# Kernel tuning notes

Measured on AMD Instinct MI355X. Metric: run time of the kernel, lower is better.

## Reference

```python
import jax, jax.numpy as jnp
import numpy as np

D_MODEL = 1024
NUM_HEADS = 16
HEAD_DIM = D_MODEL // NUM_HEADS
B, S = 2, 2048
EPS = 1e-8


def setup_inputs() -> dict:
    key = jax.random.key(0)
    ks = jax.random.split(key, 9)
    sc = 1.0 / np.sqrt(D_MODEL)
    return {
        "x": jax.random.normal(ks[0], (B, S, D_MODEL), jnp.float32),
        "wq": jax.random.normal(ks[1], (D_MODEL, D_MODEL), jnp.float32) * sc,
        "bq": jax.random.normal(ks[2], (D_MODEL,), jnp.float32) * 0.01,
        "wk": jax.random.normal(ks[3], (D_MODEL, D_MODEL), jnp.float32) * sc,
        "bk": jax.random.normal(ks[4], (D_MODEL,), jnp.float32) * 0.01,
        "wv": jax.random.normal(ks[5], (D_MODEL, D_MODEL), jnp.float32) * sc,
        "bv": jax.random.normal(ks[6], (D_MODEL,), jnp.float32) * 0.01,
        "wo": jax.random.normal(ks[7], (D_MODEL, D_MODEL), jnp.float32) * sc,
        "bo": jax.random.normal(ks[8], (D_MODEL,), jnp.float32) * 0.01,
    }


def reference(x, wq, bq, wk, bk, wv, bv, wo, bo):
    b, s, d = x.shape
    h, hd = NUM_HEADS, HEAD_DIM
    # projections (torch Linear: y = x W^T + b); reshape to [b, h, s, hd]
    def proj(w, bias):
        return (jnp.einsum('bsd,ed->bse', x, w) + bias).reshape(b, s, h, hd).transpose(0, 2, 1, 3)
    q = proj(wq, bq)
    k = proj(wk, bk)
    v = proj(wv, bv)
    scores = jnp.einsum('bhqd,bhkd->bhqk', q, k) / np.sqrt(hd)
    attn = jax.nn.softmax(scores, axis=-1)
    o = jnp.einsum('bhqk,bhkd->bhqd', attn, v)  # [b, h, s, hd]
    # per-position, per-head Gram-Schmidt exclusion: remove component of o[i]
    # along v[i] (the loop in the original is independent over positions)
    v_norm_sq = jnp.sum(v * v, axis=-1, keepdims=True)          # [b,h,s,1]
    align = jnp.sum(o * v, axis=-1, keepdims=True) / (v_norm_sq + EPS)
    o = o - align * v
    o = o.transpose(0, 2, 1, 3).reshape(b, s, d)
    return jnp.einsum('bsd,ed->bse', o, wo) + bo
```

## Files before the change

kernel.cpp:

```cpp
#include <hip/hip_runtime.h>
#include <stdint.h>

#define SEQ 2048
#define NTOK 4096
#define DM 1024

typedef __bf16 bf16x8 __attribute__((ext_vector_type(8)));
typedef __bf16 bf16x4 __attribute__((ext_vector_type(4)));
typedef float f32x4 __attribute__((ext_vector_type(4)));

__device__ __forceinline__ unsigned short f2bf(float f) {
  union { float f; unsigned u; } v; v.f = f;
  return (unsigned short)((v.u + 0x7fffu + ((v.u >> 16) & 1u)) >> 16);
}
__device__ __forceinline__ float bf2f(unsigned short s) {
  union { unsigned u; float f; } v; v.u = ((unsigned)s) << 16; return v.f;
}
__device__ __forceinline__ unsigned pkbf(float a, float b) {
  union { float f; unsigned u; } x, y; x.f = a; y.f = b;
  return __builtin_amdgcn_perm(y.u + 0x8000u, x.u + 0x8000u, 0x07060302u);
}

__device__ __forceinline__ void async16(const unsigned short* g, unsigned short* l) {
  __builtin_amdgcn_global_load_lds(
      (const __attribute__((address_space(1))) void*)g,
      (__attribute__((address_space(3))) void*)l, 16, 0, 0);
}

__global__ __launch_bounds__(256) void cast_all(
    const float* __restrict__ x, const float* __restrict__ wq,
    const float* __restrict__ wk, const float* __restrict__ wv,
    const float* __restrict__ wo, unsigned short* __restrict__ dst) {
  size_t i = ((size_t)blockIdx.x * 256 + threadIdx.x) * 4;
  const float* src; size_t off;
  if (i < (size_t)NTOK * DM) { src = x; off = i; }
  else {
    size_t j = i - (size_t)NTOK * DM;
    int s = (int)(j >> 20);
    src = (s == 0) ? wq : (s == 1) ? wk : (s == 2) ? wv : wo;
    off = j & 1048575u;
  }
  float4 f = *(const float4*)(src + off);
  ushort4 o;
  o.x = f2bf(f.x); o.y = f2bf(f.y); o.z = f2bf(f.z); o.w = f2bf(f.w);
  *(ushort4*)(dst + i) = o;
}


template<int MI>
__device__ __forceinline__ void stage_half(
    const unsigned short* __restrict__ A, const unsigned short* __restrict__ Bw,
    int m0, int n0, int kt, unsigned short* As, unsigned short* Bs) {
  const int tid = threadIdx.x;
  const int r = tid >> 2, c = tid & 3;
#pragma unroll
  for (int b = 0; b < MI / 2; ++b) {
    const int row = b * 64 + r;
    async16(A + (size_t)(m0 + row) * 1024 + kt + ((c ^ (row & 3)) << 3),
            As + row * 32 + c * 8);
  }
#pragma unroll
  for (int b = 0; b < 2; ++b) {
    const int row = b * 64 + r;
    async16(Bw + (size_t)(n0 + row) * 1024 + kt + ((c ^ (row & 3)) << 3),
            Bs + row * 32 + c * 8);
  }
}

__device__ __forceinline__ void pipe_bar0() {
  asm volatile("s_waitcnt vmcnt(0)\ns_barrier" ::: "memory");
}
template<int MI>
__device__ __forceinline__ void pipe_barN() {
  if constexpr (MI == 4) asm volatile("s_waitcnt vmcnt(4)\ns_barrier" ::: "memory");
  else                   asm volatile("s_waitcnt vmcnt(3)\ns_barrier" ::: "memory");
}

template<int MI>
__device__ __forceinline__ void gemm_pipe(
    const unsigned short* __restrict__ A, const unsigned short* __restrict__ Bw,
    int m0, int n0, f32x4 (&acc)[MI][4],
    unsigned short* AsBase, unsigned short* BsBase) {
  const int tid = threadIdx.x, lane = tid & 63, w = tid >> 6;
  const int wm16 = (w >> 1) * MI * 16, wn = (w & 1) * 64;
  const int quad = lane >> 4, l16 = lane & 15;
  constexpr int ASZ = MI * 32 * 32;
  constexpr int BSZ = 128 * 32;

  stage_half<MI>(A, Bw, m0, n0, 0,  AsBase,       BsBase);
  stage_half<MI>(A, Bw, m0, n0, 32, AsBase + ASZ, BsBase + BSZ);
  pipe_barN<MI>();

  int cur = 0;
  for (int p = 0; p < 32; ++p) {
    const unsigned short* As = AsBase + cur * ASZ;
    const unsigned short* Bs = BsBase + cur * BSZ;

    bf16x8 af[MI], bf[4];
    const int swz = ((quad ^ (l16 & 3)) << 3);
#pragma unroll
    for (int i = 0; i < MI; ++i)
      af[i] = *(const bf16x8*)(As + (wm16 + i * 16 + l16) * 32 + swz);
#pragma unroll
    for (int j = 0; j < 4; ++j)
      bf[j] = *(const bf16x8*)(Bs + (wn + j * 16 + l16) * 32 + swz);

    if (p + 2 < 32) {
      const int slot = (cur == 0) ? 2 : cur - 1;
      stage_half<MI>(A, Bw, m0, n0, (p + 2) * 32,
                     AsBase + slot * ASZ, BsBase + slot * BSZ);
    }

#pragma unroll
    for (int i = 0; i < MI; ++i)
#pragma unroll
      for (int j = 0; j < 4; ++j)
        acc[i][j] = __builtin_amdgcn_mfma_f32_16x16x32_bf16(af[i], bf[j], acc[i][j], 0, 0, 0);

    if (p < 30)       pipe_barN<MI>();
    else if (p == 30) pipe_bar0();
    cur = (cur == 2) ? 0 : cur + 1;
  }
}

__global__ __launch_bounds__(256, 3) void qkv_gemm(
    const unsigned short* __restrict__ xb,
    const unsigned short* __restrict__ wqb, const unsigned short* __restrict__ wkb,
    const unsigned short* __restrict__ wvb,
    const float* __restrict__ bq, const float* __restrict__ bk, const float* __restrict__ bv,
    unsigned short* __restrict__ Q, unsigned short* __restrict__ Kd,
    unsigned short* __restrict__ Vt) {
  __shared__ unsigned short As[3 * 128 * 32], Bs[3 * 128 * 32];
  const int gx = blockIdx.x;
  const int kind = gx >> 8;
  const int rr = gx & 255;
  const int tok = 4 * (rr & 7) + ((rr >> 3) & 3);
  const int oth = rr >> 5;
  const unsigned short* A; const unsigned short* Bw;
  int m0, n0;
  if (kind == 2) { A = wvb; Bw = xb; m0 = oth * 128; n0 = tok * 128; }
  else { A = xb; Bw = kind ? wkb : wqb; m0 = tok * 128; n0 = oth * 128; }

  f32x4 acc[4][4];
#pragma unroll
  for (int i = 0; i < 4; ++i)
#pragma unroll
    for (int j = 0; j < 4; ++j) { f32x4 z = {0.f, 0.f, 0.f, 0.f}; acc[i][j] = z; }
  gemm_pipe<4>(A, Bw, m0, n0, acc, As, Bs);

  const int lane = threadIdx.x & 63, w = threadIdx.x >> 6;
  const int quad = lane >> 4, l16 = lane & 15;
  const int wm = (w >> 1) * 64, wn = (w & 1) * 64;

  if (kind == 2) {
#pragma unroll
    for (int i = 0; i < 4; ++i)
#pragma unroll
      for (int j = 0; j < 4; ++j) {
        const int n = n0 + wn + j * 16 + l16;
        const int tb = n >> 11, s = n & 2047;
#pragma unroll
        for (int r = 0; r < 4; ++r) {
          const int m = m0 + wm + i * 16 + quad * 4 + r;
          const int h = m >> 6, d = m & 63;
          Vt[((size_t)(tb * 16 + h) * 64 + d) * SEQ + s] = f2bf(acc[i][j][r] + bv[m]);
        }
      }
  } else {
    const float* bias = (kind == 0) ? bq : bk;
    const float scale = (kind == 0) ? 0.180336880f : 1.0f;
#pragma unroll
    for (int i = 0; i < 4; ++i)
#pragma unroll
      for (int j = 0; j < 4; ++j) {
        const int col = n0 + wn + j * 16 + l16;
        const float bb = bias[col];
        const int h = col >> 6, d = col & 63;
#pragma unroll
        for (int r = 0; r < 4; ++r) {
          const int m = m0 + wm + i * 16 + quad * 4 + r;
          const int b = m >> 11, s = m & 2047;
          const int bh = b * 16 + h;
          const unsigned short val = f2bf((acc[i][j][r] + bb) * scale);
          if (kind == 0) Q[((size_t)bh * SEQ + s) * 64 + d] = val;
          else           Kd[((size_t)bh * SEQ + s) * 64 + d] = val;
        }
      }
  }
}

__global__ __launch_bounds__(256, 4) void attn_kernel(
    const unsigned short* __restrict__ Q, const unsigned short* __restrict__ Kd,
    const unsigned short* __restrict__ Vt,
    unsigned short* __restrict__ Op, float* __restrict__ Lp) {
  __shared__ unsigned short KV[4][4096];
  const int gx = blockIdx.x;
  const int xcd = gx & 7;
  const int idx = gx >> 3;
  const int bh  = xcd * 4 + (idx & 3);
  const int ksl = (idx >> 2) & 1;
  const int q0  = (idx >> 3) * 128;
  const int ks0 = ksl << 10;
  const int tid = threadIdx.x, lane = tid & 63, w = tid >> 6;
  const int quad = lane >> 4, l16 = lane & 15;
  const unsigned short* Qp = Q + (size_t)bh * SEQ * 64;
  const unsigned short* Kp = Kd + (size_t)bh * SEQ * 64;
  const unsigned short* Vp = Vt + (size_t)bh * 64 * SEQ;
  const int srow = tid >> 3;
  const int sc = ((tid & 7) ^ ((srow & 3) | ((srow & 8) >> 1))) << 3;

#pragma unroll
  for (int c = 0; c < 4; ++c)
    async16(Qp + (size_t)(q0 + c * 32 + srow) * 64 + sc,
            KV[c >> 1] + (c & 1) * 2048 + tid * 8);
  __syncthreads();

  const int gl = (l16 & 3) | ((l16 & 8) >> 1);
  const int sel = l16 & 7;
  const unsigned short* Qsrc = KV[w >> 1] + (w & 1) * 2048;
  bf16x8 bQ[2][2];
#pragma unroll
  for (int qq = 0; qq < 2; ++qq) {
    const int qrow = qq * 16 + l16;
#pragma unroll
    for (int hh = 0; hh < 2; ++hh)
      bQ[qq][hh] = *(const bf16x8*)(Qsrc + qrow * 64 + (((hh * 4 + quad) ^ gl) << 3));
  }
  __syncthreads();

  async16(Kp + (size_t)(ks0 + srow) * 64 + sc, KV[0] + tid * 8);
  async16(Kp + (size_t)(ks0 + 32 + srow) * 64 + sc, KV[0] + 2048 + tid * 8);
  async16(Vp + (size_t)srow * SEQ + ks0 + sc, KV[2] + tid * 8);
  async16(Vp + (size_t)(32 + srow) * SEQ + ks0 + sc, KV[2] + 2048 + tid * 8);

  union { unsigned short u[8]; bf16x8 v; } one8;
#pragma unroll
  for (int t = 0; t < 8; ++t) one8.u[t] = 0x3F80;
  const bf16x8 aOnes = one8.v;

  f32x4 o_acc[2][4];
  f32x4 l_acc[2];
  const f32x4 zinit = {-12.f, -12.f, -12.f, -12.f};
#pragma unroll
  for (int qq = 0; qq < 2; ++qq) {
    f32x4 z = {0.f, 0.f, 0.f, 0.f};
    l_acc[qq] = z;
#pragma unroll
    for (int dt = 0; dt < 4; ++dt) o_acc[qq][dt] = z;
  }

  for (int it = 0; it < 16; ++it) {
    const int cur = it & 1;
    __syncthreads();
    if (it + 1 < 16) {
      const int kt = ks0 + (it + 1) * 64, nb = (it + 1) & 1;
      async16(Kp + (size_t)(kt + srow) * 64 + sc, KV[nb] + tid * 8);
      async16(Kp + (size_t)(kt + 32 + srow) * 64 + sc, KV[nb] + 2048 + tid * 8);
      async16(Vp + (size_t)srow * SEQ + kt + sc, KV[2 + nb] + tid * 8);
      async16(Vp + (size_t)(32 + srow) * SEQ + kt + sc, KV[2 + nb] + 2048 + tid * 8);
    }
    const unsigned short* Ks = KV[cur];
    const unsigned short* Vs = KV[2 + cur];

    bf16x8 bP[2][2];
#pragma unroll
    for (int ee = 0; ee < 4; ++ee) {
      const int G = ee >> 1, e = ee & 1;
      const int R = G * 32 + ((l16 >> 2) << 3) + e * 4 + (l16 & 3);
      const unsigned short* arow = Ks + R * 64;
      bf16x8 a0 = *(const bf16x8*)(arow + ((quad ^ sel) << 3));
      bf16x8 a1 = *(const bf16x8*)(arow + (((4 + quad) ^ sel) << 3));
#pragma unroll
      for (int qq = 0; qq < 2; ++qq) {
        f32x4 z = __builtin_amdgcn_mfma_f32_16x16x32_bf16(a0, bQ[qq][0], zinit, 0, 0, 0);
        z = __builtin_amdgcn_mfma_f32_16x16x32_bf16(a1, bQ[qq][1], z, 0, 0, 0);
        const unsigned u0 = (unsigned)(int)__builtin_fmaf(z[0], 8388608.0f, 1065024977.0f);
        const unsigned u1 = (unsigned)(int)__builtin_fmaf(z[1], 8388608.0f, 1065024977.0f);
        const unsigned u2 = (unsigned)(int)__builtin_fmaf(z[2], 8388608.0f, 1065024977.0f);
        const unsigned u3 = (unsigned)(int)__builtin_fmaf(z[3], 8388608.0f, 1065024977.0f);
        union { unsigned d[4]; bf16x8 v; } pk;
        pk.v = bP[qq][G];
        pk.d[e * 2]     = __builtin_amdgcn_perm(u1, u0, 0x07060302u);
        pk.d[e * 2 + 1] = __builtin_amdgcn_perm(u3, u2, 0x07060302u);
        bP[qq][G] = pk.v;
      }
    }

#pragma unroll
    for (int qq = 0; qq < 2; ++qq)
#pragma unroll
      for (int G = 0; G < 2; ++G)
        l_acc[qq] = __builtin_amdgcn_mfma_f32_16x16x32_bf16(aOnes, bP[qq][G], l_acc[qq], 0, 0, 0);

#pragma unroll
    for (int dt = 0; dt < 4; ++dt) {
      const unsigned short* vbase = Vs + (dt * 16 + l16) * 64;
#pragma unroll
      for (int G = 0; G < 2; ++G) {
        bf16x8 aV = *(const bf16x8*)(vbase + (((G * 4 + quad) ^ gl) << 3));
#pragma unroll
        for (int qq = 0; qq < 2; ++qq)
          o_acc[qq][dt] = __builtin_amdgcn_mfma_f32_16x16x32_bf16(aV, bP[qq][G], o_acc[qq][dt], 0, 0, 0);
      }
    }
  }

  const size_t sb = (size_t)(ksl * 32 + bh);
#pragma unroll
  for (int qq = 0; qq < 2; ++qq) {
    const int qg = q0 + w * 32 + qq * 16 + l16;
#pragma unroll
    for (int dt = 0; dt < 4; ++dt)
#pragma unroll
      for (int r = 0; r < 4; ++r) {
        const int d = dt * 16 + quad * 4 + r;
        Op[(sb * 64 + d) * SEQ + qg] = f2bf(o_acc[qq][dt][r]);
      }
    if (quad == 0) Lp[sb * SEQ + qg] = l_acc[qq][0];
  }
}

__global__ __launch_bounds__(128) void combine_kernel(
    const unsigned short* __restrict__ Op, const float* __restrict__ Lp,
    const unsigned short* __restrict__ Vt, unsigned short* __restrict__ O) {
  const int bh = blockIdx.y;
  const int q = blockIdx.x * 128 + threadIdx.x;
  const size_t QC = (size_t)32 * SEQ;
  const size_t idx = (size_t)bh * SEQ + q;
  const float inv = 1.0f / (Lp[idx] + Lp[QC + idx]);
  const unsigned short* O1 = Op + (size_t)bh * 64 * SEQ + q;
  const unsigned short* O2 = O1 + QC * 64;
  const unsigned short* Vp = Vt + (size_t)bh * 64 * SEQ + q;
  float o64[64];
  float ov = 0.f, vv = 0.f;
#pragma unroll
  for (int d = 0; d < 64; ++d) {
    const float o = (bf2f(O1[(size_t)d * SEQ]) + bf2f(O2[(size_t)d * SEQ])) * inv;
    const float v = bf2f(Vp[(size_t)d * SEQ]);
    o64[d] = o; ov += o * v; vv += v * v;
  }
  const float align = ov / (vv + 1e-8f);
  const int b = bh >> 4, h = bh & 15;
  unsigned short* dst = O + (size_t)(b * SEQ + q) * DM + h * 64;
#pragma unroll
  for (int d = 0; d < 64; d += 2) {
    const float a0 = o64[d]     - align * bf2f(Vp[(size_t)d * SEQ]);
    const float a1 = o64[d + 1] - align * bf2f(Vp[(size_t)(d + 1) * SEQ]);
    *(unsigned*)(dst + d) = pkbf(a0, a1);
  }
}

__global__ __launch_bounds__(256) void out_gemm(
    const unsigned short* __restrict__ Ob, const unsigned short* __restrict__ wob,
    const float* __restrict__ bo, float* __restrict__ out) {
  __shared__ unsigned short As[3 * 64 * 32], Bs[3 * 128 * 32];
  const int m0 = blockIdx.y * 64, n0 = blockIdx.x * 128;
  f32x4 acc[2][4];
#pragma unroll
  for (int i = 0; i < 2; ++i)
#pragma unroll
    for (int j = 0; j < 4; ++j) { f32x4 z = {0.f, 0.f, 0.f, 0.f}; acc[i][j] = z; }

  gemm_pipe<2>(Ob, wob, m0, n0, acc, As, Bs);

  const int lane = threadIdx.x & 63, w = threadIdx.x >> 6;
  const int quad = lane >> 4, l16 = lane & 15;
  const int wm = (w >> 1) * 32, wn = (w & 1) * 64;
#pragma unroll
  for (int i = 0; i < 2; ++i)
#pragma unroll
    for (int j = 0; j < 4; ++j) {
      const int col = n0 + wn + j * 16 + l16;
      const float bb = bo[col];
#pragma unroll
      for (int r = 0; r < 4; ++r) {
        const int m = m0 + wm + i * 16 + quad * 4 + r;
        out[(size_t)m * DM + col] = acc[i][j][r] + bb;
      }
    }
}

extern "C" void kernel_launch(void* const* d_in, const int* in_sizes, int n_in,
                              void* d_out, int out_size, void* d_ws, size_t ws_size,
                              hipStream_t stream) {
  const float* x  = (const float*)d_in[0];
  const float* wq = (const float*)d_in[1];
  const float* bq = (const float*)d_in[2];
  const float* wk = (const float*)d_in[3];
  const float* bk = (const float*)d_in[4];
  const float* wv = (const float*)d_in[5];
  const float* bv = (const float*)d_in[6];
  const float* wo = (const float*)d_in[7];
  const float* bo = (const float*)d_in[8];
  float* out = (float*)d_out;
  (void)in_sizes; (void)n_in; (void)out_size; (void)ws_size;

  unsigned short* ws  = (unsigned short*)d_ws;
  unsigned short* xb  = ws;
  unsigned short* wqb = xb + (size_t)NTOK * DM;
  unsigned short* wkb = wqb + (size_t)DM * DM;
  unsigned short* wvb = wkb + (size_t)DM * DM;
  unsigned short* wob = wvb + (size_t)DM * DM;
  unsigned short* Qb  = wob + (size_t)DM * DM;
  unsigned short* Kb  = Qb + (size_t)NTOK * DM;
  unsigned short* Vtb = Kb + (size_t)NTOK * DM;
  unsigned short* Ob  = Vtb + (size_t)NTOK * DM;
  unsigned short* Opb = Ob + (size_t)NTOK * DM;
  float* Lpw = (float*)(Opb + (size_t)2 * 32 * 64 * SEQ);

  cast_all<<<8192, 256, 0, stream>>>(x, wq, wk, wv, wo, ws);
  qkv_gemm<<<768, 256, 0, stream>>>(xb, wqb, wkb, wvb, bq, bk, bv, Qb, Kb, Vtb);
  attn_kernel<<<1024, 256, 0, stream>>>(Qb, Kb, Vtb, Opb, Lpw);
  combine_kernel<<<dim3(16, 32), 128, 0, stream>>>(Opb, Lpw, Vtb, Ob);
  out_gemm<<<dim3(8, 64), 256, 0, stream>>>(Ob, wob, bo, out);
}
```

Baseline: 187.7 us.

## Double query tile per attention block and triple-buffer K/V staging

```diff
diff --git a/kernel.cpp b/kernel.cpp
--- a/kernel.cpp
+++ b/kernel.cpp
@@ -189,17 +189,17 @@
   }
 }
 
-__global__ __launch_bounds__(256, 4) void attn_kernel(
+__global__ __launch_bounds__(256, 3) void attn_kernel(
     const unsigned short* __restrict__ Q, const unsigned short* __restrict__ Kd,
     const unsigned short* __restrict__ Vt,
     unsigned short* __restrict__ Op, float* __restrict__ Lp) {
-  __shared__ unsigned short KV[4][4096];
+  __shared__ unsigned short KK[3][4096], VV[3][4096];
   const int gx = blockIdx.x;
   const int xcd = gx & 7;
   const int idx = gx >> 3;
   const int bh  = xcd * 4 + (idx & 3);
   const int ksl = (idx >> 2) & 1;
-  const int q0  = (idx >> 3) * 128;
+  const int q0  = (idx >> 3) * 256;
   const int ks0 = ksl << 10;
   const int tid = threadIdx.x, lane = tid & 63, w = tid >> 6;
   const int quad = lane >> 4, l16 = lane & 15;
@@ -210,17 +210,19 @@
   const int sc = ((tid & 7) ^ ((srow & 3) | ((srow & 8) >> 1))) << 3;
 
 #pragma unroll
-  for (int c = 0; c < 4; ++c)
-    async16(Qp + (size_t)(q0 + c * 32 + srow) * 64 + sc,
-            KV[c >> 1] + (c & 1) * 2048 + tid * 8);
+  for (int c = 0; c < 8; ++c) {
+    unsigned short* qd = (c < 6) ? (KK[c >> 1] + (c & 1) * 2048)
+                                 : (VV[0] + (c & 1) * 2048);
+    async16(Qp + (size_t)(q0 + c * 32 + srow) * 64 + sc, qd + tid * 8);
+  }
   __syncthreads();
 
   const int gl = (l16 & 3) | ((l16 & 8) >> 1);
   const int sel = l16 & 7;
-  const unsigned short* Qsrc = KV[w >> 1] + (w & 1) * 2048;
-  bf16x8 bQ[2][2];
-#pragma unroll
-  for (int qq = 0; qq < 2; ++qq) {
+  const unsigned short* Qsrc = (w < 3) ? KK[w] : VV[0];
+  bf16x8 bQ[4][2];
+#pragma unroll
+  for (int qq = 0; qq < 4; ++qq) {
     const int qrow = qq * 16 + l16;
 #pragma unroll
     for (int hh = 0; hh < 2; ++hh)
@@ -228,41 +230,40 @@
   }
   __syncthreads();
 
-  async16(Kp + (size_t)(ks0 + srow) * 64 + sc, KV[0] + tid * 8);
-  async16(Kp + (size_t)(ks0 + 32 + srow) * 64 + sc, KV[0] + 2048 + tid * 8);
-  async16(Vp + (size_t)srow * SEQ + ks0 + sc, KV[2] + tid * 8);
-  async16(Vp + (size_t)(32 + srow) * SEQ + ks0 + sc, KV[2] + 2048 + tid * 8);
+  auto stageKV = [&](int j, int slot) {
+    const int kt = ks0 + j * 64;
+    async16(Kp + (size_t)(kt + srow) * 64 + sc, KK[slot] + tid * 8);
+    async16(Kp + (size_t)(kt + 32 + srow) * 64 + sc, KK[slot] + 2048 + tid * 8);
+    async16(Vp + (size_t)srow * SEQ + kt + sc, VV[slot] + tid * 8);
+    async16(Vp + (size_t)(32 + srow) * SEQ + kt + sc, VV[slot] + 2048 + tid * 8);
+  };
+  stageKV(0, 0);
+  stageKV(1, 1);
+  asm volatile("s_waitcnt vmcnt(4)\ns_barrier" ::: "memory");
 
   union { unsigned short u[8]; bf16x8 v; } one8;
 #pragma unroll
   for (int t = 0; t < 8; ++t) one8.u[t] = 0x3F80;
   const bf16x8 aOnes = one8.v;
 
-  f32x4 o_acc[2][4];
-  f32x4 l_acc[2];
+  f32x4 o_acc[4][4];
+  f32x4 l_acc[4];
   const f32x4 zinit = {-12.f, -12.f, -12.f, -12.f};
 #pragma unroll
-  for (int qq = 0; qq < 2; ++qq) {
+  for (int qq = 0; qq < 4; ++qq) {
     f32x4 z = {0.f, 0.f, 0.f, 0.f};
     l_acc[qq] = z;
 #pragma unroll
     for (int dt = 0; dt < 4; ++dt) o_acc[qq][dt] = z;
   }
 
+  int cur = 0;
   for (int it = 0; it < 16; ++it) {
-    const int cur = it & 1;
-    __syncthreads();
-    if (it + 1 < 16) {
-      const int kt = ks0 + (it + 1) * 64, nb = (it + 1) & 1;
-      async16(Kp + (size_t)(kt + srow) * 64 + sc, KV[nb] + tid * 8);
-      async16(Kp + (size_t)(kt + 32 + srow) * 64 + sc, KV[nb] + 2048 + tid * 8);
-      async16(Vp + (size_t)srow * SEQ + kt + sc, KV[2 + nb] + tid * 8);
-      async16(Vp + (size_t)(32 + srow) * SEQ + kt + sc, KV[2 + nb] + 2048 + tid * 8);
-    }
-    const unsigned short* Ks = KV[cur];
-    const unsigned short* Vs = KV[2 + cur];
-
-    bf16x8 bP[2][2];
+    if (it + 2 < 16) stageKV(it + 2, (cur == 0) ? 2 : cur - 1);
+    const unsigned short* Ks = KK[cur];
+    const unsigned short* Vs = VV[cur];
+
+    bf16x8 bP[4][2];
 #pragma unroll
     for (int ee = 0; ee < 4; ++ee) {
       const int G = ee >> 1, e = ee & 1;
@@ -271,7 +272,7 @@
       bf16x8 a0 = *(const bf16x8*)(arow + ((quad ^ sel) << 3));
       bf16x8 a1 = *(const bf16x8*)(arow + (((4 + quad) ^ sel) << 3));
 #pragma unroll
-      for (int qq = 0; qq < 2; ++qq) {
+      for (int qq = 0; qq < 4; ++qq) {
         f32x4 z = __builtin_amdgcn_mfma_f32_16x16x32_bf16(a0, bQ[qq][0], zinit, 0, 0, 0);
         z = __builtin_amdgcn_mfma_f32_16x16x32_bf16(a1, bQ[qq][1], z, 0, 0, 0);
         const unsigned u0 = (unsigned)(int)__builtin_fmaf(z[0], 8388608.0f, 1065024977.0f);
@@ -287,7 +288,7 @@
     }
 
 #pragma unroll
-    for (int qq = 0; qq < 2; ++qq)
+    for (int qq = 0; qq < 4; ++qq)
 #pragma unroll
       for (int G = 0; G < 2; ++G)
         l_acc[qq] = __builtin_amdgcn_mfma_f32_16x16x32_bf16(aOnes, bP[qq][G], l_acc[qq], 0, 0, 0);
@@ -299,16 +300,20 @@
       for (int G = 0; G < 2; ++G) {
         bf16x8 aV = *(const bf16x8*)(vbase + (((G * 4 + quad) ^ gl) << 3));
 #pragma unroll
-        for (int qq = 0; qq < 2; ++qq)
+        for (int qq = 0; qq < 4; ++qq)
           o_acc[qq][dt] = __builtin_amdgcn_mfma_f32_16x16x32_bf16(aV, bP[qq][G], o_acc[qq][dt], 0, 0, 0);
       }
     }
+
+    if (it < 14)       asm volatile("s_waitcnt vmcnt(4)\ns_barrier" ::: "memory");
+    else if (it == 14) asm volatile("s_waitcnt vmcnt(0)\ns_barrier" ::: "memory");
+    cur = (cur == 2) ? 0 : cur + 1;
   }
 
   const size_t sb = (size_t)(ksl * 32 + bh);
 #pragma unroll
-  for (int qq = 0; qq < 2; ++qq) {
-    const int qg = q0 + w * 32 + qq * 16 + l16;
+  for (int qq = 0; qq < 4; ++qq) {
+    const int qg = q0 + w * 64 + qq * 16 + l16;
 #pragma unroll
     for (int dt = 0; dt < 4; ++dt)
 #pragma unroll
@@ -410,7 +415,7 @@
 
   cast_all<<<8192, 256, 0, stream>>>(x, wq, wk, wv, wo, ws);
   qkv_gemm<<<768, 256, 0, stream>>>(xb, wqb, wkb, wvb, bq, bk, bv, Qb, Kb, Vtb);
-  attn_kernel<<<1024, 256, 0, stream>>>(Qb, Kb, Vtb, Opb, Lpw);
+  attn_kernel<<<512, 256, 0, stream>>>(Qb, Kb, Vtb, Opb, Lpw);
   combine_kernel<<<dim3(16, 32), 128, 0, stream>>>(Opb, Lpw, Vtb, Ob);
   out_gemm<<<dim3(8, 64), 256, 0, stream>>>(Ob, wob, bo, out);
 }
```

New measurement: 195.2 us. +4.0%, slower.
